# Kernel tuning notes

Measured on AMD Instinct MI355X. Metric: run time of the kernel, lower is better.

The kernel has to match this reference:

```python
import jax, jax.numpy as jnp
import numpy as np
from jax import lax

B, S, N, FD = 4, 12, 307, 3
E = 64; F = 64; H = 64; K = 3; HEADS = 4; P = 12; DFF = 64


def setup_inputs() -> dict:
    key = jax.random.key(0)
    ks = jax.random.split(key, 24)
    rn = lambda i, shape, s=0.1: jax.random.normal(ks[i], shape, dtype=jnp.float32) * s
    z = lambda n: jnp.zeros((n,), jnp.float32)
    return {
        'x': jax.random.normal(ks[0], (B, S, N, FD), dtype=jnp.float32),
        'cheb': rn(1, (K, N, N), 0.05),
        'theta': rn(2, (K, E, F)),
        'W_emb_x': rn(3, (1, E)), 'b_emb_x': z(E),
        'W_emb_os': rn(4, (FD - 1, E)), 'b_emb_os': z(E),
        'U_x': rn(5, (F, 4 * H)), 'V_x': rn(6, (H, 4 * H)), 'b_x': z(4 * H),
        'U_g': rn(7, (F, 2 * H)), 'V_g': rn(8, (H, 2 * H)), 'b_g': z(2 * H),
        'W_ff1': rn(9, (H, DFF)), 'b_ff1': z(DFF), 'W_ff2': rn(10, (DFF, H)), 'b_ff2': z(H),
        'W_tc': rn(11, (F, H, 1, 3)), 'b_tc': z(F),
        'W_rc': rn(12, (F, H, 1, 1)), 'b_rc': z(F),
        'W_in': rn(13, (3 * F, F)), 'b_in': z(3 * F),
        'W_out': rn(14, (F, F)), 'b_out': z(F),
        'W_fa1': rn(15, (F, DFF)), 'b_fa1': z(DFF), 'W_fa2': rn(16, (DFF, F)), 'b_fa2': z(F),
        'W_fin': rn(17, (P, S, 1, F)), 'b_fin': z(P),
    }


def _forward(x, cheb, theta, W_emb_x, b_emb_x, W_emb_os, b_emb_os,
             U_x, V_x, b_x, U_g, V_g, b_g, W_ff1, b_ff1, W_ff2, b_ff2,
             W_tc, b_tc, W_rc, b_rc, W_in, b_in, W_out, b_out,
             W_fa1, b_fa1, W_fa2, b_fa2, W_fin, b_fin):
    # token embeddings (dropout=0 -> identity)
    emb_x = x[..., :1] @ W_emb_x + b_emb_x          # (B,S,N,E)
    emb_os = x[..., 1:] @ W_emb_os + b_emb_os       # (B,S,N,E)

    def cheb_conv(h):
        # sum_k relu-after-sum of T_k @ h @ theta_k
        agg = jnp.einsum('kmn,bsnc->kbsmc', cheb, h)
        return jax.nn.relu(jnp.einsum('kbsmc,kcd->bsmd', agg, theta))

    gcn_x = cheb_conv(emb_x)                        # (B,S,N,F)
    gcn_os = cheb_conv(emb_os)                      # (B,S,N,F)

    # Glstm: precompute input projections, scan the recurrence over time
    gx = jnp.einsum('bsnc,cf->sbnf', gcn_x, U_x) + b_x    # (S,B,N,4H)
    gg = jnp.einsum('bsnc,cf->sbnf', gcn_os, U_g) + b_g   # (S,B,N,2H)

    h0 = jnp.zeros((B, N, H), x.dtype)
    c0 = jnp.zeros((B, N, H), x.dtype)

    def step(carry, inp):
        ht, ct = carry
        gx_t, gg_t = inp
        gates = jax.nn.sigmoid(gx_t + ht @ V_x)     # ft,it,ot,ut all sigmoid (as in source)
        gov = jax.nn.sigmoid(gg_t + ht @ V_g)
        ft, it, ot, ut = jnp.split(gates, 4, axis=-1)
        gf, gu = jnp.split(gov, 2, axis=-1)
        ct = gf * ft * ct + gu * it * ut
        ht = ot * jnp.tanh(ct)
        return (ht, ct), ht

    _, hs = lax.scan(step, (h0, c0), (gx, gg))
    hidden = jnp.moveaxis(hs, 0, 1)                 # (B,S,N,H)
    # Muti_glstm output feedforward
    hidden = jax.nn.relu(hidden @ W_ff1 + b_ff1) @ W_ff2 + b_ff2

    # time conv: (1,3) kernel over time axis, pad 1
    hs_nchw = jnp.transpose(hidden, (0, 3, 2, 1))   # (B,H,N,S)
    tc = lax.conv_general_dilated(hs_nchw, W_tc, (1, 1), ((0, 0), (1, 1)),
                                  dimension_numbers=('NCHW', 'OIHW', 'NCHW'))
    tc = jnp.transpose(tc + b_tc[None, :, None, None], (0, 3, 2, 1))  # (B,S,N,F)

    # query = last time step, repeated over S
    query = jnp.broadcast_to(tc[:, -1:], (B, S, N, F))
    q_in = jnp.reshape(jnp.swapaxes(query, 2, 3), (B * N, S, F))
    kv_in = jnp.reshape(jnp.swapaxes(emb_x, 2, 3), (B * N, S, E))

    # torch MHA (batch_first=False): seq axis is dim0 (L=B*N), batch axis is dim1 (S)
    hd = F // HEADS
    Wq, Wk, Wv = jnp.split(W_in, 3, axis=0)
    bq, bk, bv = jnp.split(b_in, 3)

    def proj(t, Wp, bp):
        L = t.shape[0]
        p = t @ Wp.T + bp                            # (L, S, F)
        return jnp.transpose(p.reshape(L, S * HEADS, hd), (1, 0, 2))  # (S*HEADS, L, hd)

    qh = proj(q_in, Wq, bq)
    kh = proj(kv_in, Wk, bk)
    vh = proj(kv_in, Wv, bv)
    scores = jnp.einsum('hld,hmd->hlm', qh, kh) / np.float32(np.sqrt(hd))
    attn = jax.nn.softmax(scores, axis=-1)
    ctx = jnp.einsum('hlm,hmd->hld', attn, vh)       # (S*HEADS, B*N, hd)
    ctx = jnp.transpose(ctx, (1, 0, 2)).reshape(B * N, S, F)
    dsa = ctx @ W_out.T + b_out                      # (B*N, S, F)

    dsa = jnp.swapaxes(dsa.reshape(B, N, S, F), 1, 2)  # (B,S,N,F)
    ffa = jax.nn.relu(dsa @ W_fa1 + b_fa1) @ W_fa2 + b_fa2
    # residual 1x1 conv over channels of hidden
    res = jnp.einsum('bsnh,fh->bsnf', hidden, W_rc[:, :, 0, 0]) + b_rc
    comb = res + ffa                                 # (B,S,N,F)
    # final conv: channels=S, kernel (1,F) valid, then take last width index
    out = jnp.einsum('bsnf,psf->bpn', comb, W_fin[:, :, 0, :]) + b_fin[None, :, None]
    return out                                       # (B, pre_len, N)


def reference(x, cheb, theta, W_emb_x, b_emb_x, W_emb_os, b_emb_os,
              U_x, V_x, b_x, U_g, V_g, b_g, W_ff1, b_ff1, W_ff2, b_ff2,
              W_tc, b_tc, W_rc, b_rc, W_in, b_in, W_out, b_out,
              W_fa1, b_fa1, W_fa2, b_fa2, W_fin, b_fin):
    return _forward(x, cheb, theta, W_emb_x, b_emb_x, W_emb_os, b_emb_os,
                    U_x, V_x, b_x, U_g, V_g, b_g, W_ff1, b_ff1, W_ff2, b_ff2,
                    W_tc, b_tc, W_rc, b_rc, W_in, b_in, W_out, b_out,
                    W_fa1, b_fa1, W_fa2, b_fa2, W_fin, b_fin)
```

## Files before the change

### kernel.cpp

```cpp
#include <hip/hip_runtime.h>
#include <hip/hip_bf16.h>

#define BB 4
#define SS 12
#define NN 307
#define LL 1228
#define BSC 48
#define GG 48
#define WS_CX    0
#define WS_CROW  132624
#define WS_TXD   133568
#define WS_TBD   133760
#define WS_T1D   133952
#define WS_T2D   134144
#define WS_TOB   134336
#define WS_WRCT  134528
#define WS_WOT   138624
#define WS_H2    142720
#define WS_TFL   1085824
#define WS_XFL   1164416
#define WS_QH    2107520
#define WS_KH    3050624
#define WS_VH    3993728
#define WS_CTX   4936832

__global__ __launch_bounds__(256) void k1_precomp(
    const float* __restrict__ theta, const float* __restrict__ Wex,
    const float* __restrict__ bex, const float* __restrict__ Weos,
    const float* __restrict__ beos, const float* __restrict__ W_rc,
    const float* __restrict__ W_out, float* __restrict__ ws) {
  int tid = threadIdx.x;
  if (tid < 192) {
    int k = tid / 64, d = tid % 64;
    float a0 = 0.f, a1 = 0.f, a2 = 0.f, a3 = 0.f, a4 = 0.f;
    for (int c = 0; c < 64; ++c) {
      float th = theta[(k * 64 + c) * 64 + d];
      a0 = fmaf(Wex[c], th, a0);
      a1 = fmaf(bex[c], th, a1);
      a2 = fmaf(Weos[c], th, a2);
      a3 = fmaf(Weos[64 + c], th, a3);
      a4 = fmaf(beos[c], th, a4);
    }
    ws[WS_TXD + tid] = a0; ws[WS_TBD + tid] = a1; ws[WS_T1D + tid] = a2;
    ws[WS_T2D + tid] = a3; ws[WS_TOB + tid] = a4;
  }
  for (int i = tid; i < 4096; i += 256) {
    int hh = i >> 6, f = i & 63;
    ws[WS_WRCT + i] = W_rc[f * 64 + hh];
    ws[WS_WOT + i]  = W_out[f * 64 + hh];
  }
}

__global__ __launch_bounds__(320) void k2_cx(const float* __restrict__ x,
                                             const float* __restrict__ cheb,
                                             float* __restrict__ ws) {
  int k = blockIdx.x / BSC, bs = blockIdx.x % BSC;
  __shared__ float xl[921];
  for (int i = threadIdx.x; i < 921; i += 320) xl[i] = x[bs * 921 + i];
  __syncthreads();
  int m = threadIdx.x;
  if (m < NN) {
    const float* ch = cheb + (k * NN + m) * NN;
    float a0 = 0.f, a1 = 0.f, a2 = 0.f, ar = 0.f;
    for (int n = 0; n < NN; ++n) {
      float c = ch[n];
      ar += c;
      a0 = fmaf(c, xl[3 * n], a0);
      a1 = fmaf(c, xl[3 * n + 1], a1);
      a2 = fmaf(c, xl[3 * n + 2], a2);
    }
    ws[WS_CX + ((k * 3 + 0) * BSC + bs) * NN + m] = a0;
    ws[WS_CX + ((k * 3 + 1) * BSC + bs) * NN + m] = a1;
    ws[WS_CX + ((k * 3 + 2) * BSC + bs) * NN + m] = a2;
    if (bs == 0) ws[WS_CROW + k * NN + m] = ar;
  }
}

__global__ __launch_bounds__(256) void k2c_xfl(const float* __restrict__ x,
                                               const float* __restrict__ Wex,
                                               const float* __restrict__ bex,
                                               float* __restrict__ ws) {
  int idx = blockIdx.x * 256 + threadIdx.x;
  if (idx < 943104) {
    int n = idx % NN;
    int t = idx / NN;
    int e = t & 63;
    int bs = t >> 6;
    ws[WS_XFL + idx] = fmaf(x[(bs * NN + n) * 3], Wex[e], bex[e]);
  }
}

__global__ __launch_bounds__(384) void k3_scan(
    const float* __restrict__ U_x, const float* __restrict__ V_x,
    const float* __restrict__ b_x, const float* __restrict__ U_g,
    const float* __restrict__ V_g, const float* __restrict__ b_g,
    const float* __restrict__ W_ff1, const float* __restrict__ b_ff1,
    const float* __restrict__ W_ff2, const float* __restrict__ b_ff2,
    const float* __restrict__ W_tc, const float* __restrict__ b_tc,
    float* __restrict__ ws) {
  int l = blockIdx.x;
  int b = l / NN, n = l % NN;
  int tid = threadIdx.x;
  __shared__ float gcx[768], gcos[768], hsb[768], sg[256], sv[128];

  for (int idx = tid; idx < 768; idx += 384) {
    int s = idx >> 6, d = idx & 63;
    int bs = b * SS + s;
    float ax = 0.f, ao = 0.f;
#pragma unroll
    for (int k = 0; k < 3; ++k) {
      float c0 = ws[WS_CX + ((k * 3 + 0) * BSC + bs) * NN + n];
      float c1 = ws[WS_CX + ((k * 3 + 1) * BSC + bs) * NN + n];
      float c2 = ws[WS_CX + ((k * 3 + 2) * BSC + bs) * NN + n];
      float cr = ws[WS_CROW + k * NN + n];
      ax += c0 * ws[WS_TXD + k * 64 + d] + cr * ws[WS_TBD + k * 64 + d];
      ao += c1 * ws[WS_T1D + k * 64 + d] + c2 * ws[WS_T2D + k * 64 + d] +
            cr * ws[WS_TOB + k * 64 + d];
    }
    gcx[idx] = fmaxf(ax, 0.f);
    gcos[idx] = fmaxf(ao, 0.f);
  }
  __syncthreads();

  float gr[12];
  float vcol[64];
  if (tid < 256) {
#pragma unroll
    for (int s = 0; s < 12; ++s) gr[s] = b_x[tid];
    for (int c = 0; c < 64; ++c) {
      float u = U_x[c * 256 + tid];
#pragma unroll
      for (int s = 0; s < 12; ++s) gr[s] = fmaf(gcx[s * 64 + c], u, gr[s]);
    }
#pragma unroll
    for (int c = 0; c < 64; ++c) vcol[c] = V_x[c * 256 + tid];
  } else {
    int j = tid - 256;
#pragma unroll
    for (int s = 0; s < 12; ++s) gr[s] = b_g[j];
    for (int c = 0; c < 64; ++c) {
      float u = U_g[c * 128 + j];
#pragma unroll
      for (int s = 0; s < 12; ++s) gr[s] = fmaf(gcos[s * 64 + c], u, gr[s]);
    }
#pragma unroll
    for (int c = 0; c < 64; ++c) vcol[c] = V_g[c * 128 + j];
  }

  float ct = 0.f;
  for (int s = 0; s < 12; ++s) {
    float a = gr[s];
    if (s > 0) {
      const float* hp = &hsb[(s - 1) * 64];
#pragma unroll
      for (int h = 0; h < 64; ++h) a = fmaf(hp[h], vcol[h], a);
    }
    float sig = 1.f / (1.f + __expf(-a));
    if (tid < 256) sg[tid] = sig; else sv[tid - 256] = sig;
    __syncthreads();
    if (tid < 64) {
      ct = sv[tid] * sg[tid] * ct + sv[64 + tid] * sg[64 + tid] * sg[192 + tid];
      hsb[s * 64 + tid] = sg[128 + tid] * tanhf(ct);
    }
    __syncthreads();
  }

  for (int idx = tid; idx < 768; idx += 384) {
    int s = idx >> 6, d = idx & 63;
    float a = b_ff1[d];
    for (int c = 0; c < 64; ++c) a = fmaf(hsb[s * 64 + c], W_ff1[c * 64 + d], a);
    gcx[idx] = fmaxf(a, 0.f);
  }
  __syncthreads();
  for (int idx = tid; idx < 768; idx += 384) {
    int s = idx >> 6, h = idx & 63;
    float a = b_ff2[h];
    for (int d = 0; d < 64; ++d) a = fmaf(gcx[s * 64 + d], W_ff2[d * 64 + h], a);
    ws[WS_H2 + ((b * SS + s) * NN + n) * 64 + h] = a;
    gcos[idx] = a;
  }
  __syncthreads();
  if (tid < 64) {
    int f = tid;
    float a = b_tc[f];
    for (int h = 0; h < 64; ++h) {
      a = fmaf(gcos[10 * 64 + h], W_tc[(f * 64 + h) * 3 + 0], a);
      a = fmaf(gcos[11 * 64 + h], W_tc[(f * 64 + h) * 3 + 1], a);
    }
    ws[WS_TFL + (b * 64 + f) * NN + n] = a;
  }
}

__global__ __launch_bounds__(256) void k5_qkv(const float* __restrict__ W_in,
                                              const float* __restrict__ b_in,
                                              float* __restrict__ ws) {
  int blk = blockIdx.x;
  int g = blk / 77, mt = blk % 77;
  int s = g >> 2, a = g & 3;
  int m0 = mt * 16;
  __shared__ float xw[16][64], qw[16][64];
  for (int i = threadIdx.x; i < 1024; i += 256) {
    int mi = i >> 6, e = i & 63;
    int m = m0 + mi;
    if (m < LL) {
      int base = m * 768 + s * 64;
      xw[mi][e] = ws[WS_XFL + base + e];
      int bq = base / 235776;
      int off = base % 19648;
      qw[mi][e] = ws[WS_TFL + bq * 19648 + off + e];
    }
  }
  __syncthreads();
  int mi = threadIdx.x >> 4, d = threadIdx.x & 15;
  int m = m0 + mi;
  if (m < LL) {
    int f = a * 16 + d;
    float aq = b_in[f], ak = b_in[64 + f], av = b_in[128 + f];
    for (int e = 0; e < 64; ++e) {
      aq = fmaf(qw[mi][e], W_in[f * 64 + e], aq);
      ak = fmaf(xw[mi][e], W_in[(64 + f) * 64 + e], ak);
      av = fmaf(xw[mi][e], W_in[(128 + f) * 64 + e], av);
    }
    int o = (g * LL + m) * 16 + d;
    ws[WS_QH + o] = aq; ws[WS_KH + o] = ak; ws[WS_VH + o] = av;
  }
}

__global__ __launch_bounds__(512) void k6_attn(float* __restrict__ ws) {
  int blk = blockIdx.x;
  int g = blk / 10, qt = blk % 10;
  int s = g >> 2, a = g & 3;
  int tid = threadIdx.x;
  int w = tid >> 6;
  int qi = tid & 63;
  int l0 = qt * 128 + qi;
  int l1 = l0 + 64;
  bool act0 = (l0 < LL), act1 = (l1 < LL);

  __shared__ float sh[9728];
  float4* kt4 = reinterpret_cast<float4*>(sh);
  float4* vt4 = reinterpret_cast<float4*>(sh + 4096);

  float q0[16], q1[16], cx0[16], cx1[16];
  if (act0) {
    const float4* qp = reinterpret_cast<const float4*>(ws + WS_QH + (g * LL + l0) * 16);
#pragma unroll
    for (int jj = 0; jj < 4; ++jj) {
      float4 t = qp[jj];
      q0[4 * jj] = t.x * 0.25f; q0[4 * jj + 1] = t.y * 0.25f;
      q0[4 * jj + 2] = t.z * 0.25f; q0[4 * jj + 3] = t.w * 0.25f;
    }
  } else {
#pragma unroll
    for (int d = 0; d < 16; ++d) q0[d] = 0.f;
  }
  if (act1) {
    const float4* qp = reinterpret_cast<const float4*>(ws + WS_QH + (g * LL + l1) * 16);
#pragma unroll
    for (int jj = 0; jj < 4; ++jj) {
      float4 t = qp[jj];
      q1[4 * jj] = t.x * 0.25f; q1[4 * jj + 1] = t.y * 0.25f;
      q1[4 * jj + 2] = t.z * 0.25f; q1[4 * jj + 3] = t.w * 0.25f;
    }
  } else {
#pragma unroll
    for (int d = 0; d < 16; ++d) q1[d] = 0.f;
  }
#pragma unroll
  for (int d = 0; d < 16; ++d) { cx0[d] = 0.f; cx1[d] = 0.f; }
  float den0 = 0.f, den1 = 0.f;

  const float4* kb = reinterpret_cast<const float4*>(ws + WS_KH + g * LL * 16);
  const float4* vb = reinterpret_cast<const float4*>(ws + WS_VH + g * LL * 16);

  for (int mt = 0; mt < 5; ++mt) {
    int mbase = mt * 256;
    int cnt = LL - mbase; if (cnt > 256) cnt = 256;
    int nf4 = cnt * 4;
    for (int i = tid; i < nf4; i += 512) {
      kt4[i] = kb[mbase * 4 + i];
      vt4[i] = vb[mbase * 4 + i];
    }
    __syncthreads();
    int e0 = w * 32;
    int e1 = e0 + 32; if (e1 > cnt) e1 = cnt;
    for (int mi = e0; mi < e1; ++mi) {
      float4 ka = kt4[mi * 4], kbb = kt4[mi * 4 + 1];
      float4 kc = kt4[mi * 4 + 2], kd = kt4[mi * 4 + 3];
      float p0 = q0[0] * ka.x, p1 = q1[0] * ka.x;
      p0 = fmaf(q0[1], ka.y, p0);   p1 = fmaf(q1[1], ka.y, p1);
      p0 = fmaf(q0[2], ka.z, p0);   p1 = fmaf(q1[2], ka.z, p1);
      p0 = fmaf(q0[3], ka.w, p0);   p1 = fmaf(q1[3], ka.w, p1);
      p0 = fmaf(q0[4], kbb.x, p0);  p1 = fmaf(q1[4], kbb.x, p1);
      p0 = fmaf(q0[5], kbb.y, p0);  p1 = fmaf(q1[5], kbb.y, p1);
      p0 = fmaf(q0[6], kbb.z, p0);  p1 = fmaf(q1[6], kbb.z, p1);
      p0 = fmaf(q0[7], kbb.w, p0);  p1 = fmaf(q1[7], kbb.w, p1);
      p0 = fmaf(q0[8], kc.x, p0);   p1 = fmaf(q1[8], kc.x, p1);
      p0 = fmaf(q0[9], kc.y, p0);   p1 = fmaf(q1[9], kc.y, p1);
      p0 = fmaf(q0[10], kc.z, p0);  p1 = fmaf(q1[10], kc.z, p1);
      p0 = fmaf(q0[11], kc.w, p0);  p1 = fmaf(q1[11], kc.w, p1);
      p0 = fmaf(q0[12], kd.x, p0);  p1 = fmaf(q1[12], kd.x, p1);
      p0 = fmaf(q0[13], kd.y, p0);  p1 = fmaf(q1[13], kd.y, p1);
      p0 = fmaf(q0[14], kd.z, p0);  p1 = fmaf(q1[14], kd.z, p1);
      p0 = fmaf(q0[15], kd.w, p0);  p1 = fmaf(q1[15], kd.w, p1);
      float e0w = __expf(fminf(p0, 60.f));
      float e1w = __expf(fminf(p1, 60.f));
      den0 += e0w; den1 += e1w;
      float4 va = vt4[mi * 4], vbb = vt4[mi * 4 + 1];
      float4 vc = vt4[mi * 4 + 2], vd = vt4[mi * 4 + 3];
      cx0[0]  = fmaf(e0w, va.x, cx0[0]);   cx1[0]  = fmaf(e1w, va.x, cx1[0]);
      cx0[1]  = fmaf(e0w, va.y, cx0[1]);   cx1[1]  = fmaf(e1w, va.y, cx1[1]);
      cx0[2]  = fmaf(e0w, va.z, cx0[2]);   cx1[2]  = fmaf(e1w, va.z, cx1[2]);
      cx0[3]  = fmaf(e0w, va.w, cx0[3]);   cx1[3]  = fmaf(e1w, va.w, cx1[3]);
      cx0[4]  = fmaf(e0w, vbb.x, cx0[4]);  cx1[4]  = fmaf(e1w, vbb.x, cx1[4]);
      cx0[5]  = fmaf(e0w, vbb.y, cx0[5]);  cx1[5]  = fmaf(e1w, vbb.y, cx1[5]);
      cx0[6]  = fmaf(e0w, vbb.z, cx0[6]);  cx1[6]  = fmaf(e1w, vbb.z, cx1[6]);
      cx0[7]  = fmaf(e0w, vbb.w, cx0[7]);  cx1[7]  = fmaf(e1w, vbb.w, cx1[7]);
      cx0[8]  = fmaf(e0w, vc.x, cx0[8]);   cx1[8]  = fmaf(e1w, vc.x, cx1[8]);
      cx0[9]  = fmaf(e0w, vc.y, cx0[9]);   cx1[9]  = fmaf(e1w, vc.y, cx1[9]);
      cx0[10] = fmaf(e0w, vc.z, cx0[10]);  cx1[10] = fmaf(e1w, vc.z, cx1[10]);
      cx0[11] = fmaf(e0w, vc.w, cx0[11]);  cx1[11] = fmaf(e1w, vc.w, cx1[11]);
      cx0[12] = fmaf(e0w, vd.x, cx0[12]);  cx1[12] = fmaf(e1w, vd.x, cx1[12]);
      cx0[13] = fmaf(e0w, vd.y, cx0[13]);  cx1[13] = fmaf(e1w, vd.y, cx1[13]);
      cx0[14] = fmaf(e0w, vd.z, cx0[14]);  cx1[14] = fmaf(e1w, vd.z, cx1[14]);
      cx0[15] = fmaf(e0w, vd.w, cx0[15]);  cx1[15] = fmaf(e1w, vd.w, cx1[15]);
    }
    __syncthreads();
  }

  float* sden = sh;
  float* scx  = sh + 512;
#pragma unroll
  for (int ph = 0; ph < 2; ++ph) {
    sden[w * 64 + qi] = ph ? den1 : den0;
    const float* cxp = ph ? cx1 : cx0;
#pragma unroll
    for (int d = 0; d < 16; ++d) scx[(w * 64 + qi) * 17 + d] = cxp[d];
    __syncthreads();
    if (tid < 256) {
      int q2 = tid >> 2, jj = tid & 3;
      int l2 = qt * 128 + ph * 64 + q2;
      if (l2 < LL) {
        float dtot = 0.f, c0 = 0.f, c1 = 0.f, c2 = 0.f, c3 = 0.f;
#pragma unroll
        for (int u = 0; u < 8; ++u) {
          dtot += sden[u * 64 + q2];
          const float* cp = &scx[(u * 64 + q2) * 17 + jj * 4];
          c0 += cp[0]; c1 += cp[1]; c2 += cp[2]; c3 += cp[3];
        }
        float inv = 1.f / dtot;
        float* op = ws + WS_CTX + (l2 * SS + s) * 64 + a * 16 + jj * 4;
        *reinterpret_cast<float4*>(op) =
            make_float4(c0 * inv, c1 * inv, c2 * inv, c3 * inv);
      }
    }
    __syncthreads();
  }
}

__global__ __launch_bounds__(64) void k7a_comb(
    const float* __restrict__ W_fa1, const float* __restrict__ b_fa1,
    const float* __restrict__ W_fa2, const float* __restrict__ b_fa2,
    const float* __restrict__ b_rc, const float* __restrict__ b_out,
    float* __restrict__ ws) {
  int blk = blockIdx.x;
  int l = blk / SS, s = blk % SS;
  int b = l / NN, n = l % NN;
  int f = threadIdx.x;
  __shared__ float h2r[64], ctr[64], dsrL[64], trL[64];

  h2r[f] = ws[WS_H2 + ((b * SS + s) * NN + n) * 64 + f];
  ctr[f] = ws[WS_CTX + (l * SS + s) * 64 + f];
  __syncthreads();

  float dsr = b_out[f], res = b_rc[f];
  for (int q = 0; q < 64; ++q) {
    dsr = fmaf(ctr[q], ws[WS_WOT + q * 64 + f], dsr);
    res = fmaf(h2r[q], ws[WS_WRCT + q * 64 + f], res);
  }
  dsrL[f] = dsr;
  __syncthreads();

  float t = b_fa1[f];
  for (int q = 0; q < 64; ++q) t = fmaf(dsrL[q], W_fa1[q * 64 + f], t);
  trL[f] = fmaxf(t, 0.f);
  __syncthreads();

  float ff = b_fa2[f];
  for (int q = 0; q < 64; ++q) ff = fmaf(trL[q], W_fa2[q * 64 + f], ff);
  ws[WS_XFL + (l * SS + s) * 64 + f] = res + ff;
}

__global__ __launch_bounds__(320) void k7b_fin(
    const float* __restrict__ W_fin, const float* __restrict__ b_fin,
    const float* __restrict__ ws, float* __restrict__ out) {
  int blk = blockIdx.x;
  int b = blk / SS, p = blk % SS;
  int tid = threadIdx.x;
  __shared__ float wf[768];
  for (int i = tid; i < 768; i += 320) wf[i] = W_fin[p * 768 + i];
  __syncthreads();
  int n = tid;
  if (n < NN) {
    const float* cb = ws + WS_XFL + (b * NN + n) * 768;
    float a0 = 0.f, a1 = 0.f, a2 = 0.f, a3 = 0.f;
    for (int i = 0; i < 768; i += 4) {
      a0 = fmaf(cb[i], wf[i], a0);
      a1 = fmaf(cb[i + 1], wf[i + 1], a1);
      a2 = fmaf(cb[i + 2], wf[i + 2], a2);
      a3 = fmaf(cb[i + 3], wf[i + 3], a3);
    }
    out[(b * SS + p) * NN + n] = (a0 + a1) + (a2 + a3) + b_fin[p];
  }
}

extern "C" void kernel_launch(void* const* d_in, const int* in_sizes, int n_in,
                              void* d_out, int out_size, void* d_ws, size_t ws_size,
                              hipStream_t stream) {
  (void)in_sizes; (void)n_in; (void)out_size; (void)ws_size;
  const float* x     = (const float*)d_in[0];
  const float* cheb  = (const float*)d_in[1];
  const float* theta = (const float*)d_in[2];
  const float* Wex   = (const float*)d_in[3];
  const float* bex   = (const float*)d_in[4];
  const float* Weos  = (const float*)d_in[5];
  const float* beos  = (const float*)d_in[6];
  const float* U_x   = (const float*)d_in[7];
  const float* V_x   = (const float*)d_in[8];
  const float* b_x   = (const float*)d_in[9];
  const float* U_g   = (const float*)d_in[10];
  const float* V_g   = (const float*)d_in[11];
  const float* b_g   = (const float*)d_in[12];
  const float* W_ff1 = (const float*)d_in[13];
  const float* b_ff1 = (const float*)d_in[14];
  const float* W_ff2 = (const float*)d_in[15];
  const float* b_ff2 = (const float*)d_in[16];
  const float* W_tc  = (const float*)d_in[17];
  const float* b_tc  = (const float*)d_in[18];
  const float* W_rc  = (const float*)d_in[19];
  const float* b_rc  = (const float*)d_in[20];
  const float* W_in  = (const float*)d_in[21];
  const float* b_in  = (const float*)d_in[22];
  const float* W_out = (const float*)d_in[23];
  const float* b_out = (const float*)d_in[24];
  const float* W_fa1 = (const float*)d_in[25];
  const float* b_fa1 = (const float*)d_in[26];
  const float* W_fa2 = (const float*)d_in[27];
  const float* b_fa2 = (const float*)d_in[28];
  const float* W_fin = (const float*)d_in[29];
  const float* b_fin = (const float*)d_in[30];
  float* ws = (float*)d_ws;
  float* outp = (float*)d_out;

  k1_precomp<<<1, 256, 0, stream>>>(theta, Wex, bex, Weos, beos, W_rc, W_out, ws);
  k2_cx<<<144, 320, 0, stream>>>(x, cheb, ws);
  k2c_xfl<<<3684, 256, 0, stream>>>(x, Wex, bex, ws);
  k3_scan<<<1228, 384, 0, stream>>>(U_x, V_x, b_x, U_g, V_g, b_g,
                                    W_ff1, b_ff1, W_ff2, b_ff2, W_tc, b_tc, ws);
  k5_qkv<<<48 * 77, 256, 0, stream>>>(W_in, b_in, ws);
  k6_attn<<<480, 512, 0, stream>>>(ws);
  k7a_comb<<<LL * SS, 64, 0, stream>>>(W_fa1, b_fa1, W_fa2, b_fa2,
                                       b_rc, b_out, ws);
  k7b_fin<<<BB * SS, 320, 0, stream>>>(W_fin, b_fin, ws, outp);
}
```

Measured before the change: 370.5 us.

## Process four graph nodes per block in LSTM scan kernel to reuse weight registers

The scan kernel now handles four (batch,node) sequences per block instead of one, so each thread's U and V weight columns loaded into registers are reused across four sequences, and the grid shrinks from 1228 to 307 blocks. Shared-memory reads are vectorised with float4 and the cell-state update now uses 256 threads instead of 64. The goal is to amortise the per-block weight loads and synchronisation cost. In exchange, register pressure rises (gr becomes 48 floats alongside vcol[64]), which may cause spills, and 307 blocks may leave some of the GPU's compute units underused.

```diff
diff --git a/kernel.cpp b/kernel.cpp
--- a/kernel.cpp
+++ b/kernel.cpp
@@ -7,6 +7,7 @@
 #define LL 1228
 #define BSC 48
 #define GG 48
+#define NT 4
 #define WS_CX    0
 #define WS_CROW  132624
 #define WS_TXD   133568
@@ -98,13 +99,16 @@
     const float* __restrict__ W_ff2, const float* __restrict__ b_ff2,
     const float* __restrict__ W_tc, const float* __restrict__ b_tc,
     float* __restrict__ ws) {
-  int l = blockIdx.x;
-  int b = l / NN, n = l % NN;
+  int bid = blockIdx.x;
   int tid = threadIdx.x;
-  __shared__ float gcx[768], gcos[768], hsb[768], sg[256], sv[128];
-
-  for (int idx = tid; idx < 768; idx += 384) {
-    int s = idx >> 6, d = idx & 63;
+  __shared__ float gcx[NT * 768], gcos[NT * 768], hsb[NT * 768];
+  __shared__ float sg[NT * 256], sv[NT * 128];
+
+  for (int idx = tid; idx < NT * 768; idx += 384) {
+    int nt = idx / 768, r = idx - nt * 768;
+    int s = r >> 6, d = r & 63;
+    int l = bid * NT + nt;
+    int b = l / NN, n = l - b * NN;
     int bs = b * SS + s;
     float ax = 0.f, ao = 0.f;
 #pragma unroll
@@ -122,26 +126,46 @@
   }
   __syncthreads();
 
-  float gr[12];
+  float gr[NT][12];
   float vcol[64];
   if (tid < 256) {
 #pragma unroll
-    for (int s = 0; s < 12; ++s) gr[s] = b_x[tid];
-    for (int c = 0; c < 64; ++c) {
-      float u = U_x[c * 256 + tid];
-#pragma unroll
-      for (int s = 0; s < 12; ++s) gr[s] = fmaf(gcx[s * 64 + c], u, gr[s]);
+    for (int nt = 0; nt < NT; ++nt)
+#pragma unroll
+      for (int s = 0; s < 12; ++s) gr[nt][s] = b_x[tid];
+    for (int c4 = 0; c4 < 16; ++c4) {
+      float u0 = U_x[(4 * c4 + 0) * 256 + tid];
+      float u1 = U_x[(4 * c4 + 1) * 256 + tid];
+      float u2 = U_x[(4 * c4 + 2) * 256 + tid];
+      float u3 = U_x[(4 * c4 + 3) * 256 + tid];
+#pragma unroll
+      for (int nt = 0; nt < NT; ++nt)
+#pragma unroll
+        for (int s = 0; s < 12; ++s) {
+          float4 g = *reinterpret_cast<const float4*>(&gcx[nt * 768 + s * 64 + 4 * c4]);
+          gr[nt][s] = fmaf(g.x, u0, fmaf(g.y, u1, fmaf(g.z, u2, fmaf(g.w, u3, gr[nt][s]))));
+        }
     }
 #pragma unroll
     for (int c = 0; c < 64; ++c) vcol[c] = V_x[c * 256 + tid];
   } else {
     int j = tid - 256;
 #pragma unroll
-    for (int s = 0; s < 12; ++s) gr[s] = b_g[j];
-    for (int c = 0; c < 64; ++c) {
-      float u = U_g[c * 128 + j];
-#pragma unroll
-      for (int s = 0; s < 12; ++s) gr[s] = fmaf(gcos[s * 64 + c], u, gr[s]);
+    for (int nt = 0; nt < NT; ++nt)
+#pragma unroll
+      for (int s = 0; s < 12; ++s) gr[nt][s] = b_g[j];
+    for (int c4 = 0; c4 < 16; ++c4) {
+      float u0 = U_g[(4 * c4 + 0) * 128 + j];
+      float u1 = U_g[(4 * c4 + 1) * 128 + j];
+      float u2 = U_g[(4 * c4 + 2) * 128 + j];
+      float u3 = U_g[(4 * c4 + 3) * 128 + j];
+#pragma unroll
+      for (int nt = 0; nt < NT; ++nt)
+#pragma unroll
+        for (int s = 0; s < 12; ++s) {
+          float4 g = *reinterpret_cast<const float4*>(&gcos[nt * 768 + s * 64 + 4 * c4]);
+          gr[nt][s] = fmaf(g.x, u0, fmaf(g.y, u1, fmaf(g.z, u2, fmaf(g.w, u3, gr[nt][s]))));
+        }
     }
 #pragma unroll
     for (int c = 0; c < 64; ++c) vcol[c] = V_g[c * 128 + j];
@@ -149,45 +173,76 @@
 
   float ct = 0.f;
   for (int s = 0; s < 12; ++s) {
-    float a = gr[s];
+    float a[NT];
+#pragma unroll
+    for (int nt = 0; nt < NT; ++nt) a[nt] = gr[nt][s];
     if (s > 0) {
-      const float* hp = &hsb[(s - 1) * 64];
-#pragma unroll
-      for (int h = 0; h < 64; ++h) a = fmaf(hp[h], vcol[h], a);
-    }
-    float sig = 1.f / (1.f + __expf(-a));
-    if (tid < 256) sg[tid] = sig; else sv[tid - 256] = sig;
+      for (int c4 = 0; c4 < 16; ++c4) {
+#pragma unroll
+        for (int nt = 0; nt < NT; ++nt) {
+          float4 h4 = *reinterpret_cast<const float4*>(&hsb[nt * 768 + (s - 1) * 64 + 4 * c4]);
+          a[nt] = fmaf(h4.x, vcol[4 * c4], fmaf(h4.y, vcol[4 * c4 + 1],
+                  fmaf(h4.z, vcol[4 * c4 + 2], fmaf(h4.w, vcol[4 * c4 + 3], a[nt]))));
+        }
+      }
+    }
+#pragma unroll
+    for (int nt = 0; nt < NT; ++nt) {
+      float sig = 1.f / (1.f + __expf(-a[nt]));
+      if (tid < 256) sg[nt * 256 + tid] = sig;
+      else sv[nt * 128 + (tid - 256)] = sig;
+    }
     __syncthreads();
-    if (tid < 64) {
-      ct = sv[tid] * sg[tid] * ct + sv[64 + tid] * sg[64 + tid] * sg[192 + tid];
-      hsb[s * 64 + tid] = sg[128 + tid] * tanhf(ct);
+    if (tid < 256) {
+      int nt = tid >> 6, j = tid & 63;
+      ct = sv[nt * 128 + j] * sg[nt * 256 + j] * ct +
+           sv[nt * 128 + 64 + j] * sg[nt * 256 + 64 + j] * sg[nt * 256 + 192 + j];
+      hsb[nt * 768 + s * 64 + j] = sg[nt * 256 + 128 + j] * tanhf(ct);
     }
     __syncthreads();
   }
 
-  for (int idx = tid; idx < 768; idx += 384) {
-    int s = idx >> 6, d = idx & 63;
-    float a = b_ff1[d];
-    for (int c = 0; c < 64; ++c) a = fmaf(hsb[s * 64 + c], W_ff1[c * 64 + d], a);
-    gcx[idx] = fmaxf(a, 0.f);
-  }
-  __syncthreads();
-  for (int idx = tid; idx < 768; idx += 384) {
-    int s = idx >> 6, h = idx & 63;
-    float a = b_ff2[h];
-    for (int d = 0; d < 64; ++d) a = fmaf(gcx[s * 64 + d], W_ff2[d * 64 + h], a);
-    ws[WS_H2 + ((b * SS + s) * NN + n) * 64 + h] = a;
-    gcos[idx] = a;
-  }
-  __syncthreads();
-  if (tid < 64) {
-    int f = tid;
-    float a = b_tc[f];
+  for (int idx = tid; idx < NT * 768; idx += 384) {
+    int nt = idx / 768, r = idx - nt * 768;
+    int s = r >> 6, d = r & 63;
+    float acc = b_ff1[d];
+    for (int c4 = 0; c4 < 16; ++c4) {
+      float4 h4 = *reinterpret_cast<const float4*>(&hsb[nt * 768 + s * 64 + 4 * c4]);
+      acc = fmaf(h4.x, W_ff1[(4 * c4 + 0) * 64 + d],
+            fmaf(h4.y, W_ff1[(4 * c4 + 1) * 64 + d],
+            fmaf(h4.z, W_ff1[(4 * c4 + 2) * 64 + d],
+            fmaf(h4.w, W_ff1[(4 * c4 + 3) * 64 + d], acc))));
+    }
+    gcx[idx] = fmaxf(acc, 0.f);
+  }
+  __syncthreads();
+  for (int idx = tid; idx < NT * 768; idx += 384) {
+    int nt = idx / 768, r = idx - nt * 768;
+    int s = r >> 6, h = r & 63;
+    int l = bid * NT + nt;
+    int b = l / NN, n = l - b * NN;
+    float acc = b_ff2[h];
+    for (int c4 = 0; c4 < 16; ++c4) {
+      float4 t4 = *reinterpret_cast<const float4*>(&gcx[nt * 768 + s * 64 + 4 * c4]);
+      acc = fmaf(t4.x, W_ff2[(4 * c4 + 0) * 64 + h],
+            fmaf(t4.y, W_ff2[(4 * c4 + 1) * 64 + h],
+            fmaf(t4.z, W_ff2[(4 * c4 + 2) * 64 + h],
+            fmaf(t4.w, W_ff2[(4 * c4 + 3) * 64 + h], acc))));
+    }
+    ws[WS_H2 + ((b * SS + s) * NN + n) * 64 + h] = acc;
+    gcos[idx] = acc;
+  }
+  __syncthreads();
+  if (tid < 256) {
+    int nt = tid >> 6, f = tid & 63;
+    int l = bid * NT + nt;
+    int b = l / NN, n = l - b * NN;
+    float acc = b_tc[f];
     for (int h = 0; h < 64; ++h) {
-      a = fmaf(gcos[10 * 64 + h], W_tc[(f * 64 + h) * 3 + 0], a);
-      a = fmaf(gcos[11 * 64 + h], W_tc[(f * 64 + h) * 3 + 1], a);
-    }
-    ws[WS_TFL + (b * 64 + f) * NN + n] = a;
+      acc = fmaf(gcos[nt * 768 + 10 * 64 + h], W_tc[(f * 64 + h) * 3 + 0], acc);
+      acc = fmaf(gcos[nt * 768 + 11 * 64 + h], W_tc[(f * 64 + h) * 3 + 1], acc);
+    }
+    ws[WS_TFL + (b * 64 + f) * NN + n] = acc;
   }
 }
 
@@ -455,8 +510,8 @@
   k1_precomp<<<1, 256, 0, stream>>>(theta, Wex, bex, Weos, beos, W_rc, W_out, ws);
   k2_cx<<<144, 320, 0, stream>>>(x, cheb, ws);
   k2c_xfl<<<3684, 256, 0, stream>>>(x, Wex, bex, ws);
-  k3_scan<<<1228, 384, 0, stream>>>(U_x, V_x, b_x, U_g, V_g, b_g,
-                                    W_ff1, b_ff1, W_ff2, b_ff2, W_tc, b_tc, ws);
+  k3_scan<<<307, 384, 0, stream>>>(U_x, V_x, b_x, U_g, V_g, b_g,
+                                   W_ff1, b_ff1, W_ff2, b_ff2, W_tc, b_tc, ws);
   k5_qkv<<<48 * 77, 256, 0, stream>>>(W_in, b_in, ws);
   k6_attn<<<480, 512, 0, stream>>>(ws);
   k7a_comb<<<LL * SS, 64, 0, stream>>>(W_fa1, b_fa1, W_fa2, b_fa2,
```

Result: slower. 416.5 us (+12.4%).
